# Kernel tuning notes

Measured on AMD Instinct MI355X. Metric: run time of the kernel, lower is better.

## Reference

```python
import jax, jax.numpy as jnp
from jax import lax
import numpy as np

B, T, L, D, TOPK, KC = 8, 4096, 256, 128, 8, 9  # KC = ctx conv kernel size


def setup_inputs() -> dict:
    key = jax.random.key(0)
    ks = jax.random.split(key, 9)
    s = 0.05
    return {
        "x": jax.random.normal(ks[0], (B, T), jnp.float32),
        "lag_embed": jax.random.normal(ks[1], (L + 1, D), jnp.float32) * s,  # nn.Embedding(L+1, d)
        "val_w": jax.random.normal(ks[2], (D, 1), jnp.float32) * s,          # nn.Linear(1, d) weight
        "val_b": jnp.zeros((D,), jnp.float32),
        "conv_w": jax.random.normal(ks[3], (D, 1, KC), jnp.float32) * s,     # Conv1d(1, d, 9) weight (O,I,K)
        "conv_b": jnp.zeros((D,), jnp.float32),
        "ctx_w": jax.random.normal(ks[4], (D, D), jnp.float32) * s,          # ctx_proj
        "ctx_b": jnp.zeros((D,), jnp.float32),
        "wq": jax.random.normal(ks[5], (D, D), jnp.float32) * s,             # Wq (no bias)
        "wk": jax.random.normal(ks[6], (D, D), jnp.float32) * s,             # Wk (no bias)
        "bias_w": jax.random.normal(ks[7], (1, D), jnp.float32) * s,         # bias_head
        "bias_b": jnp.zeros((1,), jnp.float32),
    }


def _lag_bank(x, Lv):
    # Xlags[b, t, l] = x[b, t-(l+1)], left-padded with zeros (per docstring/intended math)
    Bv, Tv = x.shape
    pads = jnp.pad(x, ((0, 0), (Lv, 0)))
    idx = Lv - 1 + jnp.arange(Tv)[:, None] - jnp.arange(Lv)[None, :]  # (T, L)
    return pads[:, idx]  # (B, T, L)


def reference(x, lag_embed, val_w, val_b, conv_w, conv_b, ctx_w, ctx_b, wq, wk, bias_w, bias_b):
    Xlags = _lag_bank(x, L)  # (B, T, L)

    # Causal context conv: left-pad 8 zeros, Conv1d(1, D, 9, padding=0)
    xp = jnp.pad(x, ((0, 0), (KC - 1, 0)))[:, None, :]  # (B, 1, T+8)
    ctx = lax.conv_general_dilated(xp, conv_w, (1,), 'VALID',
                                   dimension_numbers=('NCH', 'OIH', 'NCH'))
    ctx = ctx + conv_b[None, :, None]           # (B, D, T)
    ctx = jnp.transpose(ctx, (0, 2, 1))         # (B, T, D)
    ctx = ctx @ ctx_w.T + ctx_b                 # ctx_proj

    q = ctx @ wq.T                              # (B, T, D)
    # score = <q, Wk Hlag> = <Wk^T q, Hlag>; Hlag = Xlags*val_w + (val_b + lag_embed[1:L+1])
    # is rank-1 in the value -> never materialize the (B,T,L,D) tensor.
    qk = q @ wk                                 # (B, T, D) = Wk^T q
    base = val_b[None, :] + lag_embed[1:L + 1]  # (L, D)
    logits = Xlags * (qk @ val_w[:, 0])[:, :, None] + qk @ base.T  # (B, T, L)

    # top-k sparsification (ties are measure-zero with continuous inputs)
    kth = lax.top_k(logits, TOPK)[0][..., -1:]
    masked = jnp.where(logits >= kth, logits, -jnp.inf)
    w = jax.nn.softmax(masked, axis=-1)         # (B, T, L)

    mu = jnp.sum(w * Xlags, axis=-1) + (ctx @ bias_w.T)[..., 0] + bias_b[0]  # (B, T)
    return mu, w
```

## Files before the change

kernel.cpp:

```cpp
#include <hip/hip_runtime.h>
#include <math.h>

#define D   128
#define LQ  256
#define KCQ 9
#define BQ  8
#define TQ  4096
#define RISK_DELTA 2e-5f
#define WCAP 16384

__global__ void pk1(const float* __restrict__ wk, const float* __restrict__ wq,
                    const float* __restrict__ ctx_w, const float* __restrict__ bias_w,
                    const float* __restrict__ conv_w, const float* __restrict__ val_b,
                    const float* __restrict__ lag_embed,
                    double* __restrict__ T2, double* __restrict__ u, int* __restrict__ wcnt,
                    float* __restrict__ ctx_wT, float* __restrict__ wqT,
                    float* __restrict__ conv_wT, float* __restrict__ baseT) {
    int tid = threadIdx.x;
    int bid = blockIdx.x;
    if (bid < D) {
        int d = bid;
        if (tid < D) {
            double acc = 0.0;
            for (int j = 0; j < D; ++j)
                acc += (double)wk[j * D + d] * (double)wq[j * D + tid];
            T2[d * D + tid] = acc;
            ctx_wT[d * D + tid] = ctx_w[tid * D + d];
            wqT[d * D + tid]    = wq[tid * D + d];
            if (d < KCQ) conv_wT[d * D + tid] = conv_w[tid * KCQ + d];
        }
        baseT[d * LQ + tid] = __fadd_rn(val_b[d], lag_embed[(size_t)(tid + 1) * D + d]);
    } else if (bid == D) {
        if (tid < D) {
            double acc = 0.0;
            for (int dd = 0; dd < D; ++dd)
                acc += (double)bias_w[dd] * (double)ctx_w[dd * D + tid];
            u[tid] = acc;
        }
    } else {
        if (tid == 0) *wcnt = 0;
    }
}

__global__ void pk2(const double* __restrict__ T2, const float* __restrict__ ctx_w,
                    const float* __restrict__ conv_w, const float* __restrict__ conv_b,
                    const float* __restrict__ ctx_b,
                    double* __restrict__ g, double* __restrict__ c1) {
    __shared__ double row[D];
    int d = blockIdx.x, e = threadIdx.x;
    double acc = 0.0;
    for (int j = 0; j < D; ++j)
        acc += T2[d * D + j] * (double)ctx_w[j * D + e];
    row[e] = acc;
    __syncthreads();
    if (e < KCQ) {
        double a = 0.0;
        for (int q = 0; q < D; ++q) a += row[q] * (double)conv_w[q * KCQ + e];
        g[e * D + d] = a;
    } else if (e == KCQ) {
        double a = 0.0;
        for (int q = 0; q < D; ++q) a += row[q] * (double)conv_b[q];
        for (int q = 0; q < D; ++q) a += T2[d * D + q] * (double)ctx_b[q];
        c1[d] = a;
    }
}

__global__ void pk3(const float* __restrict__ lag_embed, const float* __restrict__ val_b,
                    const float* __restrict__ val_w, const float* __restrict__ conv_w,
                    const float* __restrict__ conv_b, const float* __restrict__ ctx_b,
                    const float* __restrict__ bias_w, const float* __restrict__ bias_b,
                    const double* __restrict__ g, const double* __restrict__ c1,
                    const double* __restrict__ u,
                    float* __restrict__ gbTf, float* __restrict__ cbvf, float* __restrict__ cstf) {
    int tid = threadIdx.x;
    if (blockIdx.x < LQ) {
        __shared__ double bl[D];
        int l = blockIdx.x;
        bl[tid] = (double)val_b[tid] + (double)lag_embed[(l + 1) * D + tid];
        __syncthreads();
        if (tid < KCQ) {
            double a = 0.0;
            for (int q = 0; q < D; ++q) a += bl[q] * g[tid * D + q];
            gbTf[tid * LQ + l] = (float)a;
        } else if (tid == KCQ) {
            double a = 0.0;
            for (int q = 0; q < D; ++q) a += bl[q] * c1[q];
            cbvf[l] = (float)a;
        }
    } else {
        if (tid < KCQ) {
            double a = 0.0, a2 = 0.0;
            for (int q = 0; q < D; ++q) a  += g[tid * D + q] * (double)val_w[q];
            for (int q = 0; q < D; ++q) a2 += u[q] * (double)conv_w[q * KCQ + tid];
            cstf[tid]      = (float)a;
            cstf[10 + tid] = (float)a2;
        } else if (tid == KCQ) {
            double a = 0.0, a2 = 0.0;
            for (int q = 0; q < D; ++q) a  += c1[q] * (double)val_w[q];
            for (int q = 0; q < D; ++q) a2 += u[q] * (double)conv_b[q];
            for (int q = 0; q < D; ++q) a2 += (double)bias_w[q] * (double)ctx_b[q];
            cstf[9]  = (float)a;
            cstf[19] = (float)(a2 + (double)bias_b[0]);
        }
    }
}

__global__ __launch_bounds__(256, 8) void lag_main(
    const float* __restrict__ x, const float* __restrict__ gbTf,
    const float* __restrict__ cbvf, const float* __restrict__ cstf,
    float* __restrict__ muOut, float* __restrict__ wOut,
    int* __restrict__ wcnt, int* __restrict__ wlist) {
    __shared__ float sgb[KCQ * LQ];
    __shared__ float scb[LQ];
    __shared__ float sc[20];
    int tid = threadIdx.x;
    #pragma unroll
    for (int i = 0; i < KCQ; ++i) sgb[i * LQ + tid] = gbTf[i * LQ + tid];
    scb[tid] = cbvf[tid];
    if (tid < 20) sc[tid] = cstf[tid];
    __syncthreads();

    int wave = tid >> 6, lane = tid & 63;
    int row = blockIdx.x * 4 + wave;
    int b = row >> 12;
    int t = row & (TQ - 1);
    const float* xb = x + b * TQ;

    float xw[KCQ];
    #pragma unroll
    for (int k = 0; k < KCQ; ++k) {
        int idx = t - 8 + k;
        xw[k] = (idx >= 0) ? xb[idx] : 0.f;
    }
    float s = sc[9], bias = sc[19];
    #pragma unroll
    for (int k = 0; k < KCQ; ++k) {
        s    = fmaf(sc[k],      xw[k], s);
        bias = fmaf(sc[10 + k], xw[k], bias);
    }

    int l0 = lane * 4;
    float xlag[4];
    #pragma unroll
    for (int i = 0; i < 4; ++i) {
        int idx = t - 1 - (l0 + i);
        xlag[i] = (idx >= 0) ? xb[idx] : 0.f;
    }

    float4 cb4 = *reinterpret_cast<const float4*>(&scb[l0]);
    float lg[4] = {cb4.x, cb4.y, cb4.z, cb4.w};
    #pragma unroll
    for (int k = 0; k < KCQ; ++k) {
        float4 g4 = *reinterpret_cast<const float4*>(&sgb[k * LQ + l0]);
        lg[0] = fmaf(g4.x, xw[k], lg[0]);
        lg[1] = fmaf(g4.y, xw[k], lg[1]);
        lg[2] = fmaf(g4.z, xw[k], lg[2]);
        lg[3] = fmaf(g4.w, xw[k], lg[3]);
    }
    #pragma unroll
    for (int i = 0; i < 4; ++i) lg[i] = fmaf(xlag[i], s, lg[i]);

    const float NEG_INF = -__builtin_inff();
    float wl0 = lg[0], wl1 = lg[1], wl2 = lg[2], wl3 = lg[3];
    float mx = 0.f, thr = 0.f, v9 = 0.f;
    #pragma unroll
    for (int it = 0; it < 9; ++it) {
        float lm = fmaxf(fmaxf(wl0, wl1), fmaxf(wl2, wl3));
        float m = lm;
        #pragma unroll
        for (int off = 32; off >= 1; off >>= 1)
            m = fmaxf(m, __shfl_xor(m, off, 64));
        if (it == 0) mx = m;
        if (it == 7) thr = m;
        if (it == 8) v9 = m;
        if (it < 8) {
            wl0 = (wl0 == m) ? NEG_INF : wl0;
            wl1 = (wl1 == m) ? NEG_INF : wl1;
            wl2 = (wl2 == m) ? NEG_INF : wl2;
            wl3 = (wl3 == m) ? NEG_INF : wl3;
        }
    }

    if ((thr - v9) < RISK_DELTA) {
        if (lane == 0) {
            int pos = atomicAdd(wcnt, 1);
            if (pos < WCAP) wlist[pos] = row;
        }
        return;
    }

    float p[4], psum = 0.f, pmu = 0.f;
    #pragma unroll
    for (int j = 0; j < 4; ++j) {
        p[j] = (lg[j] >= thr) ? __expf(lg[j] - mx) : 0.f;
        psum += p[j];
        pmu = fmaf(p[j], xlag[j], pmu);
    }
    #pragma unroll
    for (int off = 32; off >= 1; off >>= 1) {
        psum += __shfl_xor(psum, off, 64);
        pmu  += __shfl_xor(pmu,  off, 64);
    }
    float inv = 1.f / psum;
    float4 wo = make_float4(p[0] * inv, p[1] * inv, p[2] * inv, p[3] * inv);
    *reinterpret_cast<float4*>(&wOut[(size_t)row * LQ + l0]) = wo;
    if (lane == 0) muOut[row] = fmaf(pmu, inv, bias);
}

__global__ __launch_bounds__(512) void fixer(
    const float* __restrict__ x, const float* __restrict__ wk,
    const float* __restrict__ val_w, const float* __restrict__ conv_b,
    const float* __restrict__ ctx_b, const float* __restrict__ bias_w,
    const float* __restrict__ bias_b,
    const float* __restrict__ ctx_wT, const float* __restrict__ wqT,
    const float* __restrict__ conv_wT, const float* __restrict__ baseT,
    const int* __restrict__ wcnt, const int* __restrict__ wlist,
    float* __restrict__ muOut, float* __restrict__ wOut) {
    __shared__ float sxw[8][KCQ];
    __shared__ float sctxc[8][D];
    __shared__ float sctxp[8][D];
    __shared__ float sq[8][D];
    __shared__ float sqk[8][D];
    __shared__ float ssv[8];
    __shared__ float sbd[8];
    __shared__ float slog[8][LQ];
    __shared__ int   srow[8];

    int cnt = *wcnt;
    if (cnt > WCAP) cnt = WCAP;
    int ngroups = (cnt + 7) >> 3;
    int tid = threadIdx.x;

    for (int gi = blockIdx.x; gi < ngroups; gi += gridDim.x) {
        if (tid < 8) {
            int idx = gi * 8 + tid;
            if (idx >= cnt) idx = cnt - 1;
            srow[tid] = wlist[idx];
        }
        __syncthreads();
        if (tid < 8 * KCQ) {
            int g = tid / KCQ, k = tid % KCQ;
            int row = srow[g]; int b = row >> 12, t = row & (TQ - 1);
            int ii = t - 8 + k;
            sxw[g][k] = (ii >= 0) ? x[b * TQ + ii] : 0.f;
        }
        __syncthreads();

        {
            int d = tid & (D - 1), r = (tid >> 7) & 3;
            float cw[KCQ];
            #pragma unroll
            for (int k = 0; k < KCQ; ++k) cw[k] = conv_wT[k * D + d];
            float a0 = 0.f, a1 = 0.f;
            #pragma unroll
            for (int k = 0; k < KCQ; ++k) {
                a0 = fmaf(cw[k], sxw[r][k], a0);
                a1 = fmaf(cw[k], sxw[r + 4][k], a1);
            }
            float cb = conv_b[d];
            sctxc[r][d]     = __fadd_rn(a0, cb);
            sctxc[r + 4][d] = __fadd_rn(a1, cb);
        }
        __syncthreads();

        {
            int e = tid & (D - 1), r = (tid >> 7) & 3;
            float a0 = 0.f, a1 = 0.f;
            float wv0[16], wv1[16];
            #pragma unroll
            for (int u = 0; u < 16; ++u) wv0[u] = ctx_wT[u * D + e];
            #pragma unroll 1
            for (int d2 = 0; d2 < D; d2 += 32) {
                #pragma unroll
                for (int u = 0; u < 16; ++u) wv1[u] = ctx_wT[(d2 + 16 + u) * D + e];
                #pragma unroll
                for (int u = 0; u < 16; ++u) {
                    a0 = fmaf(wv0[u], sctxc[r][d2 + u], a0);
                    a1 = fmaf(wv0[u], sctxc[r + 4][d2 + u], a1);
                }
                if (d2 + 32 < D) {
                    #pragma unroll
                    for (int u = 0; u < 16; ++u) wv0[u] = ctx_wT[(d2 + 32 + u) * D + e];
                }
                #pragma unroll
                for (int u = 0; u < 16; ++u) {
                    a0 = fmaf(wv1[u], sctxc[r][d2 + 16 + u], a0);
                    a1 = fmaf(wv1[u], sctxc[r + 4][d2 + 16 + u], a1);
                }
            }
            float cb = ctx_b[e];
            sctxp[r][e]     = __fadd_rn(a0, cb);
            sctxp[r + 4][e] = __fadd_rn(a1, cb);
        }
        __syncthreads();

        {
            int e = tid & (D - 1), r = (tid >> 7) & 3;
            float a0 = 0.f, a1 = 0.f;
            float wv0[16], wv1[16];
            #pragma unroll
            for (int u = 0; u < 16; ++u) wv0[u] = wqT[u * D + e];
            #pragma unroll 1
            for (int e2 = 0; e2 < D; e2 += 32) {
                #pragma unroll
                for (int u = 0; u < 16; ++u) wv1[u] = wqT[(e2 + 16 + u) * D + e];
                #pragma unroll
                for (int u = 0; u < 16; ++u) {
                    a0 = fmaf(wv0[u], sctxp[r][e2 + u], a0);
                    a1 = fmaf(wv0[u], sctxp[r + 4][e2 + u], a1);
                }
                if (e2 + 32 < D) {
                    #pragma unroll
                    for (int u = 0; u < 16; ++u) wv0[u] = wqT[(e2 + 32 + u) * D + e];
                }
                #pragma unroll
                for (int u = 0; u < 16; ++u) {
                    a0 = fmaf(wv1[u], sctxp[r][e2 + 16 + u], a0);
                    a1 = fmaf(wv1[u], sctxp[r + 4][e2 + 16 + u], a1);
                }
            }
            sq[r][e]     = a0;
            sq[r + 4][e] = a1;
        }
        __syncthreads();

        {
            int e = tid & (D - 1), r = (tid >> 7) & 3;
            float a0 = 0.f, a1 = 0.f;
            float wv0[16], wv1[16];
            #pragma unroll
            for (int u = 0; u < 16; ++u) wv0[u] = wk[u * D + e];
            #pragma unroll 1
            for (int a2i = 0; a2i < D; a2i += 32) {
                #pragma unroll
                for (int u = 0; u < 16; ++u) wv1[u] = wk[(a2i + 16 + u) * D + e];
                #pragma unroll
                for (int u = 0; u < 16; ++u) {
                    a0 = fmaf(wv0[u], sq[r][a2i + u], a0);
                    a1 = fmaf(wv0[u], sq[r + 4][a2i + u], a1);
                }
                if (a2i + 32 < D) {
                    #pragma unroll
                    for (int u = 0; u < 16; ++u) wv0[u] = wk[(a2i + 32 + u) * D + e];
                }
                #pragma unroll
                for (int u = 0; u < 16; ++u) {
                    a0 = fmaf(wv1[u], sq[r][a2i + 16 + u], a0);
                    a1 = fmaf(wv1[u], sq[r + 4][a2i + 16 + u], a1);
                }
            }
            sqk[r][e]     = a0;
            sqk[r + 4][e] = a1;
        }
        __syncthreads();

        if (tid < 8) {
            int g = tid;
            float a = 0.f;
            #pragma unroll 1
            for (int d2 = 0; d2 < D; d2 += 16) {
                float vv[16];
                #pragma unroll
                for (int u = 0; u < 16; ++u) vv[u] = val_w[d2 + u];
                #pragma unroll
                for (int u = 0; u < 16; ++u) a = fmaf(sqk[g][d2 + u], vv[u], a);
            }
            ssv[g] = a;
        } else if (tid < 16) {
            int g = tid - 8;
            float a = 0.f;
            #pragma unroll 1
            for (int e2 = 0; e2 < D; e2 += 16) {
                float vv[16];
                #pragma unroll
                for (int u = 0; u < 16; ++u) vv[u] = bias_w[e2 + u];
                #pragma unroll
                for (int u = 0; u < 16; ++u) a = fmaf(sctxp[g][e2 + u], vv[u], a);
            }
            sbd[g] = a;
        }
        __syncthreads();

        {
            int l = tid & (LQ - 1);
            int h = tid >> 8;
            int r0 = h * 4;
            float c0 = 0.f, c1v = 0.f, c2 = 0.f, c3 = 0.f;
            float bd0[16], bd1[16];
            #pragma unroll
            for (int u = 0; u < 16; ++u) bd0[u] = baseT[u * LQ + l];
            #pragma unroll 1
            for (int d2 = 0; d2 < D; d2 += 32) {
                #pragma unroll
                for (int u = 0; u < 16; ++u) bd1[u] = baseT[(d2 + 16 + u) * LQ + l];
                #pragma unroll
                for (int u = 0; u < 16; ++u) {
                    float bd = bd0[u];
                    c0  = fmaf(bd, sqk[r0 + 0][d2 + u], c0);
                    c1v = fmaf(bd, sqk[r0 + 1][d2 + u], c1v);
                    c2  = fmaf(bd, sqk[r0 + 2][d2 + u], c2);
                    c3  = fmaf(bd, sqk[r0 + 3][d2 + u], c3);
                }
                if (d2 + 32 < D) {
                    #pragma unroll
                    for (int u = 0; u < 16; ++u) bd0[u] = baseT[(d2 + 32 + u) * LQ + l];
                }
                #pragma unroll
                for (int u = 0; u < 16; ++u) {
                    float bd = bd1[u];
                    c0  = fmaf(bd, sqk[r0 + 0][d2 + 16 + u], c0);
                    c1v = fmaf(bd, sqk[r0 + 1][d2 + 16 + u], c1v);
                    c2  = fmaf(bd, sqk[r0 + 2][d2 + 16 + u], c2);
                    c3  = fmaf(bd, sqk[r0 + 3][d2 + 16 + u], c3);
                }
            }
            float accs[4] = {c0, c1v, c2, c3};
            #pragma unroll
            for (int j = 0; j < 4; ++j) {
                int g = r0 + j;
                int row = srow[g]; int b = row >> 12, t = row & (TQ - 1);
                int ii = t - 1 - l;
                float xl = (ii >= 0) ? x[b * TQ + ii] : 0.f;
                slog[g][l] = __fadd_rn(__fmul_rn(xl, ssv[g]), accs[j]);
            }
        }
        __syncthreads();

        {
            int wv = tid >> 6, lane = tid & 63;
            int gg = wv;
            float lv0 = slog[gg][lane], lv1 = slog[gg][lane + 64];
            float lv2 = slog[gg][lane + 128], lv3 = slog[gg][lane + 192];
            const float NEG_INF = -__builtin_inff();
            float w0 = lv0, w1 = lv1, w2 = lv2, w3 = lv3;
            float mx = 0.f, thr = 0.f;
            #pragma unroll
            for (int it = 0; it < 8; ++it) {
                float lm = fmaxf(fmaxf(w0, w1), fmaxf(w2, w3));
                float m = lm;
                #pragma unroll
                for (int off = 32; off >= 1; off >>= 1)
                    m = fmaxf(m, __shfl_xor(m, off, 64));
                if (it == 0) mx = m;
                thr = m;
                if (it < 7) {
                    unsigned long long ball = __ballot(lm == m);
                    int leader = __ffsll(ball) - 1;
                    if (lane == leader) {
                        if (w0 == m)      w0 = NEG_INF;
                        else if (w1 == m) w1 = NEG_INF;
                        else if (w2 == m) w2 = NEG_INF;
                        else              w3 = NEG_INF;
                    }
                }
            }
            int row = srow[gg]; int b = row >> 12, t = row & (TQ - 1);
            float p[4], xlg[4];
            double ps = 0.0;
            float lvs[4] = {lv0, lv1, lv2, lv3};
            #pragma unroll
            for (int j = 0; j < 4; ++j) {
                int l = lane + 64 * j;
                int ii = t - 1 - l;
                xlg[j] = (ii >= 0) ? x[b * TQ + ii] : 0.f;
                p[j] = (lvs[j] >= thr) ? (float)exp((double)__fsub_rn(lvs[j], mx)) : 0.f;
                ps += (double)p[j];
            }
            #pragma unroll
            for (int off = 32; off >= 1; off >>= 1)
                ps += __shfl_xor(ps, off, 64);
            float psf = (float)ps;
            double mud = 0.0;
            #pragma unroll
            for (int j = 0; j < 4; ++j) {
                float wvv = __fdiv_rn(p[j], psf);
                wOut[(size_t)row * LQ + lane + 64 * j] = wvv;
                mud += (double)__fmul_rn(wvv, xlg[j]);
            }
            #pragma unroll
            for (int off = 32; off >= 1; off >>= 1)
                mud += __shfl_xor(mud, off, 64);
            if (lane == 0) {
                float m1 = (float)mud;
                m1 = __fadd_rn(m1, sbd[gg]);
                m1 = __fadd_rn(m1, bias_b[0]);
                muOut[row] = m1;
            }
        }
        __syncthreads();
    }
}

extern "C" void kernel_launch(void* const* d_in, const int* in_sizes, int n_in,
                              void* d_out, int out_size, void* d_ws, size_t ws_size,
                              hipStream_t stream) {
    const float* x         = (const float*)d_in[0];
    const float* lag_embed = (const float*)d_in[1];
    const float* val_w     = (const float*)d_in[2];
    const float* val_b     = (const float*)d_in[3];
    const float* conv_w    = (const float*)d_in[4];
    const float* conv_b    = (const float*)d_in[5];
    const float* ctx_w     = (const float*)d_in[6];
    const float* ctx_b     = (const float*)d_in[7];
    const float* wq        = (const float*)d_in[8];
    const float* wk        = (const float*)d_in[9];
    const float* bias_w    = (const float*)d_in[10];
    const float* bias_b    = (const float*)d_in[11];

    char* wsb = (char*)d_ws;
    double* T2  = (double*)wsb;
    double* g   = T2 + 16384;
    double* u   = g + 1152;
    double* c1  = u + 128;
    float* gbTf = (float*)(c1 + 128);
    float* cbvf = gbTf + 2304;
    float* cstf = cbvf + 256;
    int* wcnt  = (int*)(wsb + 163840);
    int* wlist = wcnt + 1;
    float* ctx_wT  = (float*)(wsb + 229504);
    float* wqT     = ctx_wT + 16384;
    float* conv_wT = wqT + 16384;
    float* baseT   = conv_wT + 1152;

    float* muOut = (float*)d_out;
    float* wOut  = muOut + BQ * TQ;

    hipLaunchKernelGGL(pk1, dim3(D + 2), dim3(256), 0, stream,
                       wk, wq, ctx_w, bias_w, conv_w, val_b, lag_embed,
                       T2, u, wcnt, ctx_wT, wqT, conv_wT, baseT);
    hipLaunchKernelGGL(pk2, dim3(D), dim3(D), 0, stream, T2, ctx_w, conv_w, conv_b, ctx_b, g, c1);
    hipLaunchKernelGGL(pk3, dim3(LQ + 1), dim3(D), 0, stream,
                       lag_embed, val_b, val_w, conv_w, conv_b, ctx_b, bias_w, bias_b,
                       g, c1, u, gbTf, cbvf, cstf);
    hipLaunchKernelGGL(lag_main, dim3(BQ * TQ / 4), dim3(256), 0, stream,
                       x, gbTf, cbvf, cstf, muOut, wOut, wcnt, wlist);
    hipLaunchKernelGGL(fixer, dim3(256), dim3(512), 0, stream,
                       x, wk, val_w, conv_b, ctx_b, bias_w, bias_b,
                       ctx_wT, wqT, conv_wT, baseT, wcnt, wlist, muOut, wOut);
}
```

Before: 96.30 us.

## Fuse pk1/pk2 precompute kernels and process several rows per lag_main block

Merges the T2 and g/c1 precompute kernels into one, keeping each T2 row in shared memory instead of writing and re-reading it from global, which removes one launch. lag_main now handles four groups of rows per block in a loop, so the shared-memory staging of gb/cb constants is amortised over more rows and the grid shrinks by four. Overflow handling changes so that a row is only deferred when the fixer list has room, otherwise it is computed inline. The cost is fewer blocks available to hide latency and a serial loop per block.

```diff
diff --git a/kernel.cpp b/kernel.cpp
--- a/kernel.cpp
+++ b/kernel.cpp
@@ -8,14 +8,19 @@
 #define TQ  4096
 #define RISK_DELTA 2e-5f
 #define WCAP 16384
-
-__global__ void pk1(const float* __restrict__ wk, const float* __restrict__ wq,
-                    const float* __restrict__ ctx_w, const float* __restrict__ bias_w,
-                    const float* __restrict__ conv_w, const float* __restrict__ val_b,
-                    const float* __restrict__ lag_embed,
-                    double* __restrict__ T2, double* __restrict__ u, int* __restrict__ wcnt,
-                    float* __restrict__ ctx_wT, float* __restrict__ wqT,
-                    float* __restrict__ conv_wT, float* __restrict__ baseT) {
+#define QPB 4
+
+__global__ void pk12(const float* __restrict__ wk, const float* __restrict__ wq,
+                     const float* __restrict__ ctx_w, const float* __restrict__ bias_w,
+                     const float* __restrict__ conv_w, const float* __restrict__ conv_b,
+                     const float* __restrict__ ctx_b, const float* __restrict__ val_b,
+                     const float* __restrict__ lag_embed,
+                     double* __restrict__ u, int* __restrict__ wcnt,
+                     double* __restrict__ g, double* __restrict__ c1,
+                     float* __restrict__ ctx_wT, float* __restrict__ wqT,
+                     float* __restrict__ conv_wT, float* __restrict__ baseT) {
+    __shared__ double dT2[D];
+    __shared__ double rowM[D];
     int tid = threadIdx.x;
     int bid = blockIdx.x;
     if (bid < D) {
@@ -24,12 +29,30 @@
             double acc = 0.0;
             for (int j = 0; j < D; ++j)
                 acc += (double)wk[j * D + d] * (double)wq[j * D + tid];
-            T2[d * D + tid] = acc;
+            dT2[tid] = acc;
             ctx_wT[d * D + tid] = ctx_w[tid * D + d];
             wqT[d * D + tid]    = wq[tid * D + d];
             if (d < KCQ) conv_wT[d * D + tid] = conv_w[tid * KCQ + d];
         }
         baseT[d * LQ + tid] = __fadd_rn(val_b[d], lag_embed[(size_t)(tid + 1) * D + d]);
+        __syncthreads();
+        if (tid < D) {
+            double acc = 0.0;
+            for (int j = 0; j < D; ++j)
+                acc += dT2[j] * (double)ctx_w[j * D + tid];
+            rowM[tid] = acc;
+        }
+        __syncthreads();
+        if (tid < KCQ) {
+            double a = 0.0;
+            for (int q = 0; q < D; ++q) a += rowM[q] * (double)conv_w[q * KCQ + tid];
+            g[tid * D + d] = a;
+        } else if (tid == KCQ) {
+            double a = 0.0;
+            for (int q = 0; q < D; ++q) a += rowM[q] * (double)conv_b[q];
+            for (int q = 0; q < D; ++q) a += dT2[q] * (double)ctx_b[q];
+            c1[d] = a;
+        }
     } else if (bid == D) {
         if (tid < D) {
             double acc = 0.0;
@@ -39,29 +62,6 @@
         }
     } else {
         if (tid == 0) *wcnt = 0;
-    }
-}
-
-__global__ void pk2(const double* __restrict__ T2, const float* __restrict__ ctx_w,
-                    const float* __restrict__ conv_w, const float* __restrict__ conv_b,
-                    const float* __restrict__ ctx_b,
-                    double* __restrict__ g, double* __restrict__ c1) {
-    __shared__ double row[D];
-    int d = blockIdx.x, e = threadIdx.x;
-    double acc = 0.0;
-    for (int j = 0; j < D; ++j)
-        acc += T2[d * D + j] * (double)ctx_w[j * D + e];
-    row[e] = acc;
-    __syncthreads();
-    if (e < KCQ) {
-        double a = 0.0;
-        for (int q = 0; q < D; ++q) a += row[q] * (double)conv_w[q * KCQ + e];
-        g[e * D + d] = a;
-    } else if (e == KCQ) {
-        double a = 0.0;
-        for (int q = 0; q < D; ++q) a += row[q] * (double)conv_b[q];
-        for (int q = 0; q < D; ++q) a += T2[d * D + q] * (double)ctx_b[q];
-        c1[d] = a;
     }
 }
 
@@ -121,90 +121,98 @@
     __syncthreads();
 
     int wave = tid >> 6, lane = tid & 63;
-    int row = blockIdx.x * 4 + wave;
-    int b = row >> 12;
-    int t = row & (TQ - 1);
-    const float* xb = x + b * TQ;
-
-    float xw[KCQ];
-    #pragma unroll
-    for (int k = 0; k < KCQ; ++k) {
-        int idx = t - 8 + k;
-        xw[k] = (idx >= 0) ? xb[idx] : 0.f;
+    int l0 = lane * 4;
+    const float4 cb4 = *reinterpret_cast<const float4*>(&scb[l0]);
+    const float NEG_INF = -__builtin_inff();
+
+    #pragma unroll 1
+    for (int it0 = 0; it0 < QPB; ++it0) {
+        int row = (blockIdx.x * QPB + it0) * 4 + wave;
+        int b = row >> 12;
+        int t = row & (TQ - 1);
+        const float* xb = x + b * TQ;
+
+        float xw[KCQ];
+        #pragma unroll
+        for (int k = 0; k < KCQ; ++k) {
+            int idx = t - 8 + k;
+            xw[k] = (idx >= 0) ? xb[idx] : 0.f;
+        }
+        float s = sc[9], bias = sc[19];
+        #pragma unroll
+        for (int k = 0; k < KCQ; ++k) {
+            s    = fmaf(sc[k],      xw[k], s);
+            bias = fmaf(sc[10 + k], xw[k], bias);
+        }
+
+        float xlag[4];
+        #pragma unroll
+        for (int i = 0; i < 4; ++i) {
+            int idx = t - 1 - (l0 + i);
+            xlag[i] = (idx >= 0) ? xb[idx] : 0.f;
+        }
+
+        float lg[4] = {cb4.x, cb4.y, cb4.z, cb4.w};
+        #pragma unroll
+        for (int k = 0; k < KCQ; ++k) {
+            float4 g4 = *reinterpret_cast<const float4*>(&sgb[k * LQ + l0]);
+            lg[0] = fmaf(g4.x, xw[k], lg[0]);
+            lg[1] = fmaf(g4.y, xw[k], lg[1]);
+            lg[2] = fmaf(g4.z, xw[k], lg[2]);
+            lg[3] = fmaf(g4.w, xw[k], lg[3]);
+        }
+        #pragma unroll
+        for (int i = 0; i < 4; ++i) lg[i] = fmaf(xlag[i], s, lg[i]);
+
+        float wl0 = lg[0], wl1 = lg[1], wl2 = lg[2], wl3 = lg[3];
+        float mx = 0.f, thr = 0.f, v9 = 0.f;
+        #pragma unroll
+        for (int it = 0; it < 9; ++it) {
+            float lm = fmaxf(fmaxf(wl0, wl1), fmaxf(wl2, wl3));
+            float m = lm;
+            #pragma unroll
+            for (int off = 32; off >= 1; off >>= 1)
+                m = fmaxf(m, __shfl_xor(m, off, 64));
+            if (it == 0) mx = m;
+            if (it == 7) thr = m;
+            if (it == 8) v9 = m;
+            if (it < 8) {
+                wl0 = (wl0 == m) ? NEG_INF : wl0;
+                wl1 = (wl1 == m) ? NEG_INF : wl1;
+                wl2 = (wl2 == m) ? NEG_INF : wl2;
+                wl3 = (wl3 == m) ? NEG_INF : wl3;
+            }
+        }
+
+        bool defer = false;
+        if ((thr - v9) < RISK_DELTA) {
+            int pos = 0;
+            if (lane == 0) pos = atomicAdd(wcnt, 1);
+            pos = __shfl(pos, 0, 64);
+            if (pos < WCAP) {
+                if (lane == 0) wlist[pos] = row;
+                defer = true;
+            }
+        }
+        if (!defer) {
+            float p[4], psum = 0.f, pmu = 0.f;
+            #pragma unroll
+            for (int j = 0; j < 4; ++j) {
+                p[j] = (lg[j] >= thr) ? __expf(lg[j] - mx) : 0.f;
+                psum += p[j];
+                pmu = fmaf(p[j], xlag[j], pmu);
+            }
+            #pragma unroll
+            for (int off = 32; off >= 1; off >>= 1) {
+                psum += __shfl_xor(psum, off, 64);
+                pmu  += __shfl_xor(pmu,  off, 64);
+            }
+            float inv = 1.f / psum;
+            float4 wo = make_float4(p[0] * inv, p[1] * inv, p[2] * inv, p[3] * inv);
+            *reinterpret_cast<float4*>(&wOut[(size_t)row * LQ + l0]) = wo;
+            if (lane == 0) muOut[row] = fmaf(pmu, inv, bias);
+        }
     }
-    float s = sc[9], bias = sc[19];
-    #pragma unroll
-    for (int k = 0; k < KCQ; ++k) {
-        s    = fmaf(sc[k],      xw[k], s);
-        bias = fmaf(sc[10 + k], xw[k], bias);
-    }
-
-    int l0 = lane * 4;
-    float xlag[4];
-    #pragma unroll
-    for (int i = 0; i < 4; ++i) {
-        int idx = t - 1 - (l0 + i);
-        xlag[i] = (idx >= 0) ? xb[idx] : 0.f;
-    }
-
-    float4 cb4 = *reinterpret_cast<const float4*>(&scb[l0]);
-    float lg[4] = {cb4.x, cb4.y, cb4.z, cb4.w};
-    #pragma unroll
-    for (int k = 0; k < KCQ; ++k) {
-        float4 g4 = *reinterpret_cast<const float4*>(&sgb[k * LQ + l0]);
-        lg[0] = fmaf(g4.x, xw[k], lg[0]);
-        lg[1] = fmaf(g4.y, xw[k], lg[1]);
-        lg[2] = fmaf(g4.z, xw[k], lg[2]);
-        lg[3] = fmaf(g4.w, xw[k], lg[3]);
-    }
-    #pragma unroll
-    for (int i = 0; i < 4; ++i) lg[i] = fmaf(xlag[i], s, lg[i]);
-
-    const float NEG_INF = -__builtin_inff();
-    float wl0 = lg[0], wl1 = lg[1], wl2 = lg[2], wl3 = lg[3];
-    float mx = 0.f, thr = 0.f, v9 = 0.f;
-    #pragma unroll
-    for (int it = 0; it < 9; ++it) {
-        float lm = fmaxf(fmaxf(wl0, wl1), fmaxf(wl2, wl3));
-        float m = lm;
-        #pragma unroll
-        for (int off = 32; off >= 1; off >>= 1)
-            m = fmaxf(m, __shfl_xor(m, off, 64));
-        if (it == 0) mx = m;
-        if (it == 7) thr = m;
-        if (it == 8) v9 = m;
-        if (it < 8) {
-            wl0 = (wl0 == m) ? NEG_INF : wl0;
-            wl1 = (wl1 == m) ? NEG_INF : wl1;
-            wl2 = (wl2 == m) ? NEG_INF : wl2;
-            wl3 = (wl3 == m) ? NEG_INF : wl3;
-        }
-    }
-
-    if ((thr - v9) < RISK_DELTA) {
-        if (lane == 0) {
-            int pos = atomicAdd(wcnt, 1);
-            if (pos < WCAP) wlist[pos] = row;
-        }
-        return;
-    }
-
-    float p[4], psum = 0.f, pmu = 0.f;
-    #pragma unroll
-    for (int j = 0; j < 4; ++j) {
-        p[j] = (lg[j] >= thr) ? __expf(lg[j] - mx) : 0.f;
-        psum += p[j];
-        pmu = fmaf(p[j], xlag[j], pmu);
-    }
-    #pragma unroll
-    for (int off = 32; off >= 1; off >>= 1) {
-        psum += __shfl_xor(psum, off, 64);
-        pmu  += __shfl_xor(pmu,  off, 64);
-    }
-    float inv = 1.f / psum;
-    float4 wo = make_float4(p[0] * inv, p[1] * inv, p[2] * inv, p[3] * inv);
-    *reinterpret_cast<float4*>(&wOut[(size_t)row * LQ + l0]) = wo;
-    if (lane == 0) muOut[row] = fmaf(pmu, inv, bias);
 }
 
 __global__ __launch_bounds__(512) void fixer(
@@ -525,14 +533,13 @@
     float* muOut = (float*)d_out;
     float* wOut  = muOut + BQ * TQ;
 
-    hipLaunchKernelGGL(pk1, dim3(D + 2), dim3(256), 0, stream,
-                       wk, wq, ctx_w, bias_w, conv_w, val_b, lag_embed,
-                       T2, u, wcnt, ctx_wT, wqT, conv_wT, baseT);
-    hipLaunchKernelGGL(pk2, dim3(D), dim3(D), 0, stream, T2, ctx_w, conv_w, conv_b, ctx_b, g, c1);
+    hipLaunchKernelGGL(pk12, dim3(D + 2), dim3(256), 0, stream,
+                       wk, wq, ctx_w, bias_w, conv_w, conv_b, ctx_b, val_b, lag_embed,
+                       u, wcnt, g, c1, ctx_wT, wqT, conv_wT, baseT);
     hipLaunchKernelGGL(pk3, dim3(LQ + 1), dim3(D), 0, stream,
                        lag_embed, val_b, val_w, conv_w, conv_b, ctx_b, bias_w, bias_b,
                        g, c1, u, gbTf, cbvf, cstf);
-    hipLaunchKernelGGL(lag_main, dim3(BQ * TQ / 4), dim3(256), 0, stream,
+    hipLaunchKernelGGL(lag_main, dim3(BQ * TQ / (4 * QPB)), dim3(256), 0, stream,
                        x, gbTf, cbvf, cstf, muOut, wOut, wcnt, wlist);
     hipLaunchKernelGGL(fixer, dim3(256), dim3(512), 0, stream,
                        x, wk, val_w, conv_b, ctx_b, bias_w, bias_b,
```

Result: slower. 158.4 us (+64.5%).
